# Performance work log

Hardware: AMD Instinct MI355X
Metric: run time of the kernel (lower is better)

Reference implementation:

```python
import jax, jax.numpy as jnp
import numpy as np

H = 16  # num_heads
D = 64  # depth per head


def setup_inputs() -> dict:
    key = jax.random.key(0)
    ks = jax.random.split(key, 9)
    hd = H * D
    s = 1.0 / np.sqrt(hd)
    return {
        "x": jax.random.normal(ks[0], (2, 2048, hd), dtype=jnp.float32),
        "wq_w": jax.random.normal(ks[1], (hd, hd), dtype=jnp.float32) * s,
        "wq_b": jnp.zeros((hd,), dtype=jnp.float32),
        "wk_w": jax.random.normal(ks[2], (hd, hd), dtype=jnp.float32) * s,
        "wk_b": jnp.zeros((hd,), dtype=jnp.float32),
        "wv_w": jax.random.normal(ks[3], (hd, hd), dtype=jnp.float32) * s,
        "wv_b": jnp.zeros((hd,), dtype=jnp.float32),
        "fc_w": jax.random.normal(ks[4], (hd, hd), dtype=jnp.float32) * s,
        "fc_b": jnp.zeros((hd,), dtype=jnp.float32),
    }


def reference(x, wq_w, wq_b, wk_w, wk_b, wv_w, wv_b, fc_w, fc_b):
    B, S, HD = x.shape
    # Linear layers (torch Linear: y = x @ W^T + b)
    q = x @ wq_w.T + wq_b
    k = x @ wk_w.T + wk_b
    v = x @ wv_w.T + wv_b
    # split heads -> [B, H, S, D]
    split = lambda t: t.reshape(B, S, H, D).transpose(0, 2, 1, 3)
    q, k, v = split(q), split(k), split(v)
    scale = 1.0 / jnp.sqrt(jnp.float32(D))
    logits = jnp.einsum("bhqd,bhkd->bhqk", q, k) * scale
    attn = jax.nn.softmax(logits, axis=-1)
    out = jnp.einsum("bhqk,bhkd->bhqd", attn, v)
    out = out.transpose(0, 2, 1, 3).reshape(B, S, HD)
    return out @ fc_w.T + fc_b
```

## Files before the change

### kernel.cpp

```cpp
#include <hip/hip_runtime.h>
#include <hip/hip_bf16.h>

typedef __hip_bfloat16 bf16;
typedef __attribute__((ext_vector_type(8))) short bf16x8;
typedef __attribute__((ext_vector_type(4))) float f32x4;
typedef __attribute__((ext_vector_type(16))) float f32x16;

static constexpr int SEQ = 2048;
static constexpr int HDIM = 1024;
static constexpr int NH = 16;
static constexpr int DH = 64;

__device__ __forceinline__ f32x4 mfma16(bf16x8 a, bf16x8 b, f32x4 c) {
  return __builtin_amdgcn_mfma_f32_16x16x32_bf16(a, b, c, 0, 0, 0);
}
__device__ __forceinline__ f32x16 mfma32(bf16x8 a, bf16x8 b, f32x16 c) {
  return __builtin_amdgcn_mfma_f32_32x32x16_bf16(a, b, c, 0, 0, 0);
}

__device__ __forceinline__ void gload_lds16(const bf16* g, bf16* l) {
  __builtin_amdgcn_global_load_lds(
      (const __attribute__((address_space(1))) void*)g,
      (__attribute__((address_space(3))) void*)l, 16, 0, 0);
}

__device__ __forceinline__ unsigned packbf(float a, float b) {
  unsigned short ua = __builtin_bit_cast(unsigned short, __float2bfloat16(a));
  unsigned short ub = __builtin_bit_cast(unsigned short, __float2bfloat16(b));
  return (unsigned)ua | ((unsigned)ub << 16);
}

__global__ __launch_bounds__(256) void cvt_bf16(const float* __restrict__ in,
                                                bf16* __restrict__ out, int n4) {
  int i = blockIdx.x * blockDim.x + threadIdx.x;
  if (i >= n4) return;
  float4 v = reinterpret_cast<const float4*>(in)[i];
  bf16 t[4] = {__float2bfloat16(v.x), __float2bfloat16(v.y),
               __float2bfloat16(v.z), __float2bfloat16(v.w)};
  reinterpret_cast<ushort4*>(out)[i] = *reinterpret_cast<ushort4*>(t);
}

__device__ __forceinline__ void gemm_core(const bf16* __restrict__ A,
                                          const bf16* __restrict__ W,
                                          int m0, int n0, int K,
                                          f32x4 (&acc)[4][4],
                                          bf16* As, bf16* Bs) {
  const int tid = threadIdx.x;
  const int w = tid >> 6, lane = tid & 63;
  const int wr = w >> 1, wc = w & 1;
  const int lr = lane & 15, lk = (lane >> 4) * 8;
  const int srow = lane >> 2, scol = (lane & 3) * 8;

  for (int kt = 0; kt < K; kt += 32) {
#pragma unroll
    for (int j = 0; j < 2; ++j) {
      int cidx = w * 2 + j;
      int r = cidx * 16 + srow;
      gload_lds16(A + (size_t)(m0 + r) * K + kt + scol, As + cidx * 512);
      gload_lds16(W + (size_t)(n0 + r) * K + kt + scol, Bs + cidx * 512);
    }
    __syncthreads();
    bf16x8 af[4], bw[4];
#pragma unroll
    for (int i = 0; i < 4; ++i)
      af[i] = *reinterpret_cast<const bf16x8*>(As + (wr * 64 + i * 16 + lr) * 32 + lk);
#pragma unroll
    for (int i = 0; i < 4; ++i)
      bw[i] = *reinterpret_cast<const bf16x8*>(Bs + (wc * 64 + i * 16 + lr) * 32 + lk);
#pragma unroll
    for (int r = 0; r < 4; ++r)
#pragma unroll
      for (int c = 0; c < 4; ++c)
        acc[r][c] = mfma16(af[r], bw[c], acc[r][c]);
    __syncthreads();
  }
}

__global__ __launch_bounds__(256)
void qkv_gemm(const bf16* __restrict__ xb,
              const bf16* __restrict__ wq, const bf16* __restrict__ wk,
              const bf16* __restrict__ wv,
              const float* __restrict__ bq, const float* __restrict__ bk,
              const float* __restrict__ bv,
              bf16* __restrict__ qd, bf16* __restrict__ kd, bf16* __restrict__ vT) {
  __shared__ bf16 As[128 * 32], Bs[128 * 32];
  const int z = blockIdx.z;
  const bf16* W = (z == 0) ? wq : (z == 1) ? wk : wv;
  const float* bias = (z == 0) ? bq : (z == 1) ? bk : bv;
  const float scale = (z == 0) ? 0.18033688011f : 1.0f;
  const int m0 = blockIdx.y * 128, n0 = blockIdx.x * 128;
  f32x4 acc[4][4] = {};
  gemm_core(xb, W, m0, n0, HDIM, acc, As, Bs);

  const int tid = threadIdx.x, w = tid >> 6, lane = tid & 63;
  const int wr = w >> 1, wc = w & 1;
  const int lr = lane & 15, rg = (lane >> 4) * 4;
#pragma unroll
  for (int r = 0; r < 4; ++r)
#pragma unroll
    for (int c = 0; c < 4; ++c) {
      int n = n0 + wc * 64 + c * 16 + lr;
      int h = n >> 6, d = n & 63;
      float bz = bias[n];
#pragma unroll
      for (int q = 0; q < 4; ++q) {
        int m = m0 + wr * 64 + r * 16 + rg + q;
        int b = m >> 11, s = m & 2047;
        bf16 val = __float2bfloat16((acc[r][c][q] + bz) * scale);
        if (z == 2)
          vT[(((size_t)(b * NH + h) * DH + d) << 11) + s] = val;
        else {
          bf16* dst = (z == 0) ? qd : kd;
          dst[(((size_t)(b * NH + h) * SEQ + s) << 6) + d] = val;
        }
      }
    }
}

__global__ __launch_bounds__(512, 4)
void attn_kernel(const bf16* __restrict__ Q, const bf16* __restrict__ K,
                 const bf16* __restrict__ vT, bf16* __restrict__ AO) {
  __shared__ float Olds[4][32][64];
  __shared__ float mlds[4][32], llds[4][32];
  __shared__ float als[8][32];
  __shared__ float af1[4][32], af2[4][32], li[4][32];

  const int lane = threadIdx.x & 63;
  const int wv = threadIdx.x >> 6;
  const int qw = wv & 3, kh = wv >> 2;
  const int l31 = lane & 31;
  const int hi = lane >> 5;
  const int bh = blockIdx.y;
  const int b = bh >> 4, h = bh & 15;
  const int q0 = blockIdx.x * 128 + qw * 32;

  const bf16* Qh = Q + (size_t)bh * SEQ * DH;
  const bf16* Kh = K + (size_t)bh * SEQ * DH;
  const bf16* Vh = vT + (size_t)bh * DH * SEQ;

  bf16x8 qf[4];
#pragma unroll
  for (int s = 0; s < 4; ++s)
    qf[s] = *reinterpret_cast<const bf16x8*>(
        Qh + (size_t)(q0 + l31) * DH + s * 16 + hi * 8);

  f32x16 o0 = {}, o1 = {};
  float m = -1e30f, l = 0.f;

  const int k_lo = kh << 10, k_hi = k_lo + 1024;
  for (int kt = k_lo; kt < k_hi; kt += 32) {
    f32x16 sacc = {};
#pragma unroll
    for (int s = 0; s < 4; ++s) {
      bf16x8 kf = *reinterpret_cast<const bf16x8*>(
          Kh + (size_t)(kt + l31) * DH + s * 16 + hi * 8);
      sacc = mfma32(kf, qf[s], sacc);
    }
    bf16x8 vf[2][2];
#pragma unroll
    for (int kk = 0; kk < 2; ++kk)
#pragma unroll
      for (int t = 0; t < 2; ++t)
        vf[kk][t] = *reinterpret_cast<const bf16x8*>(
            Vh + (size_t)(t * 32 + l31) * SEQ + kt + kk * 16 + hi * 8);

    float tm[8];
#pragma unroll
    for (int i = 0; i < 8; ++i) tm[i] = fmaxf(sacc[2 * i], sacc[2 * i + 1]);
#pragma unroll
    for (int i = 0; i < 4; ++i) tm[i] = fmaxf(tm[i], tm[i + 4]);
    float pmax = fmaxf(fmaxf(tm[0], tm[1]), fmaxf(tm[2], tm[3]));
    pmax = fmaxf(pmax, __shfl_xor(pmax, 32));

    if (__any(pmax > m + 11.5415603f)) {
      float mn = fmaxf(m, pmax);
      float al = exp2f(m - mn);
      m = mn; l *= al;
      if (lane < 32) als[wv][l31] = al;
      __builtin_amdgcn_wave_barrier();
#pragma unroll
      for (int r = 0; r < 16; ++r) {
        float a = als[wv][(r & 3) + 8 * (r >> 2) + 4 * hi];
        o0[r] *= a; o1[r] *= a;
      }
      __builtin_amdgcn_wave_barrier();
    }

    float p[16];
#pragma unroll
    for (int i = 0; i < 16; ++i) p[i] = exp2f(sacc[i] - m);
    float ts[8];
#pragma unroll
    for (int i = 0; i < 8; ++i) ts[i] = p[2 * i] + p[2 * i + 1];
#pragma unroll
    for (int i = 0; i < 4; ++i) ts[i] = ts[i] + ts[i + 4];
    float ps = (ts[0] + ts[1]) + (ts[2] + ts[3]);
    ps += __shfl_xor(ps, 32);
    l += ps;

    unsigned w[4][2], sw[4][2];
#pragma unroll
    for (int g = 0; g < 4; ++g) {
      w[g][0] = packbf(p[4 * g + 0], p[4 * g + 1]);
      w[g][1] = packbf(p[4 * g + 2], p[4 * g + 3]);
      sw[g][0] = __shfl_xor(w[g][0], 32);
      sw[g][1] = __shfl_xor(w[g][1], 32);
    }
#pragma unroll
    for (int kk = 0; kk < 2; ++kk) {
      union { unsigned u[4]; bf16x8 v; } fa;
      fa.u[0] = hi ? sw[2 * kk + 1][0] : w[2 * kk][0];
      fa.u[1] = hi ? sw[2 * kk + 1][1] : w[2 * kk][1];
      fa.u[2] = hi ? w[2 * kk + 1][0] : sw[2 * kk][0];
      fa.u[3] = hi ? w[2 * kk + 1][1] : sw[2 * kk][1];
      o0 = mfma32(fa.v, vf[kk][0], o0);
      o1 = mfma32(fa.v, vf[kk][1], o1);
    }
  }

  if (kh == 1) {
    if (lane < 32) { mlds[qw][l31] = m; llds[qw][l31] = l; }
#pragma unroll
    for (int r = 0; r < 16; ++r) {
      int q = (r & 3) + 8 * (r >> 2) + 4 * hi;
      Olds[qw][q][l31] = o0[r];
      Olds[qw][q][32 + l31] = o1[r];
    }
  }
  __syncthreads();
  if (kh == 0) {
    float m2 = mlds[qw][l31], l2 = llds[qw][l31];
    float mn = fmaxf(m, m2);
    float a1 = exp2f(m - mn), a2 = exp2f(m2 - mn);
    float inv = 1.0f / (l * a1 + l2 * a2);
    if (lane < 32) { af1[qw][l31] = a1; af2[qw][l31] = a2; li[qw][l31] = inv; }
    __builtin_amdgcn_wave_barrier();
#pragma unroll
    for (int r = 0; r < 16; ++r) {
      int q = (r & 3) + 8 * (r >> 2) + 4 * hi;
      float s1 = af1[qw][q], s2 = af2[qw][q], iv = li[qw][q];
      size_t row = (size_t)(b * SEQ + q0 + q) * HDIM + h * DH;
      AO[row + l31] =
          __float2bfloat16((o0[r] * s1 + Olds[qw][q][l31] * s2) * iv);
      AO[row + 32 + l31] =
          __float2bfloat16((o1[r] * s1 + Olds[qw][q][32 + l31] * s2) * iv);
    }
  }
}

__global__ __launch_bounds__(256)
void fc_gemm(const bf16* __restrict__ A, const bf16* __restrict__ W,
             const float* __restrict__ bias, float* __restrict__ out) {
  __shared__ bf16 As[128 * 32], Bs[128 * 32];
  const int m0 = blockIdx.y * 128, n0 = blockIdx.x * 128;
  f32x4 acc[4][4] = {};
  gemm_core(A, W, m0, n0, HDIM, acc, As, Bs);

  const int tid = threadIdx.x, w = tid >> 6, lane = tid & 63;
  const int wr = w >> 1, wc = w & 1;
  const int lr = lane & 15, rg = (lane >> 4) * 4;
#pragma unroll
  for (int r = 0; r < 4; ++r)
#pragma unroll
    for (int c = 0; c < 4; ++c) {
      int n = n0 + wc * 64 + c * 16 + lr;
      float bz = bias[n];
#pragma unroll
      for (int q = 0; q < 4; ++q) {
        int m = m0 + wr * 64 + r * 16 + rg + q;
        out[(size_t)m * HDIM + n] = acc[r][c][q] + bz;
      }
    }
}

extern "C" void kernel_launch(void* const* d_in, const int* in_sizes, int n_in,
                              void* d_out, int out_size, void* d_ws, size_t ws_size,
                              hipStream_t stream) {
  (void)in_sizes; (void)n_in; (void)out_size; (void)ws_size;
  const float* x  = (const float*)d_in[0];
  const float* wq = (const float*)d_in[1];
  const float* bq = (const float*)d_in[2];
  const float* wk = (const float*)d_in[3];
  const float* bk = (const float*)d_in[4];
  const float* wv = (const float*)d_in[5];
  const float* bv = (const float*)d_in[6];
  const float* wf = (const float*)d_in[7];
  const float* bf_ = (const float*)d_in[8];
  float* out = (float*)d_out;

  char* ws = (char*)d_ws;
  bf16* xb  = (bf16*)(ws);
  bf16* wqb = (bf16*)(ws + (8u << 20));
  bf16* wkb = (bf16*)(ws + (10u << 20));
  bf16* wvb = (bf16*)(ws + (12u << 20));
  bf16* wfb = (bf16*)(ws + (14u << 20));
  bf16* qd  = (bf16*)(ws + (16u << 20));
  bf16* kd  = (bf16*)(ws + (24u << 20));
  bf16* vT  = (bf16*)(ws + (32u << 20));
  bf16* ao  = (bf16*)(ws + (40u << 20));

  cvt_bf16<<<4096, 256, 0, stream>>>(x, xb, 1048576);
  cvt_bf16<<<1024, 256, 0, stream>>>(wq, wqb, 262144);
  cvt_bf16<<<1024, 256, 0, stream>>>(wk, wkb, 262144);
  cvt_bf16<<<1024, 256, 0, stream>>>(wv, wvb, 262144);
  cvt_bf16<<<1024, 256, 0, stream>>>(wf, wfb, 262144);

  qkv_gemm<<<dim3(8, 32, 3), 256, 0, stream>>>(xb, wqb, wkb, wvb, bq, bk, bv,
                                               qd, kd, vT);
  attn_kernel<<<dim3(16, 32), 512, 0, stream>>>(qd, kd, vT, ao);
  fc_gemm<<<dim3(8, 32), 256, 0, stream>>>(ao, wfb, bf_, out);
}
```

Before: 274.1 us.

## Use packed bf16 convert and permlane swap in attention; merge weight conversions

The four weight conversion launches become one launch that picks its input by blockIdx.z, removing three kernel launches. In the attention inner loop, the per-element bf16 packing and cross-half shuffles with selects are replaced by v_cvt_pk_bf16_f32 and v_permlane32_swap_b32 inline assembly. The row max is rebuilt from three-input max trees, and the K/V addresses now come from incremented pointers instead of per-iteration index maths. The gain is fewer VALU and cross-lane instructions per tile, at the cost of relying on gfx950-specific instructions and inline asm whose operand order must reproduce the previous fragment layout.

```diff
diff --git a/kernel.cpp b/kernel.cpp
--- a/kernel.cpp
+++ b/kernel.cpp
@@ -24,16 +24,43 @@
       (__attribute__((address_space(3))) void*)l, 16, 0, 0);
 }
 
-__device__ __forceinline__ unsigned packbf(float a, float b) {
-  unsigned short ua = __builtin_bit_cast(unsigned short, __float2bfloat16(a));
-  unsigned short ub = __builtin_bit_cast(unsigned short, __float2bfloat16(b));
-  return (unsigned)ua | ((unsigned)ub << 16);
+__device__ __forceinline__ unsigned cvtpk(float lo, float hi) {
+  unsigned r;
+  asm("v_cvt_pk_bf16_f32 %0, %1, %2" : "=v"(r) : "v"(lo), "v"(hi));
+  return r;
+}
+__device__ __forceinline__ void plswap(unsigned& a, unsigned& b) {
+  asm volatile("v_permlane32_swap_b32 %0, %1" : "+v"(a), "+v"(b));
+}
+__device__ __forceinline__ float xhalf_max(float x) {
+  return fmaxf(x, __shfl_xor(x, 32));
+}
+__device__ __forceinline__ float xhalf_sum(float x) {
+  return x + __shfl_xor(x, 32);
+}
+__device__ __forceinline__ float max3f(float a, float b, float c) {
+  return fmaxf(fmaxf(a, b), c);
 }
 
 __global__ __launch_bounds__(256) void cvt_bf16(const float* __restrict__ in,
                                                 bf16* __restrict__ out, int n4) {
   int i = blockIdx.x * blockDim.x + threadIdx.x;
   if (i >= n4) return;
+  float4 v = reinterpret_cast<const float4*>(in)[i];
+  bf16 t[4] = {__float2bfloat16(v.x), __float2bfloat16(v.y),
+               __float2bfloat16(v.z), __float2bfloat16(v.w)};
+  reinterpret_cast<ushort4*>(out)[i] = *reinterpret_cast<ushort4*>(t);
+}
+
+__global__ __launch_bounds__(256)
+void cvt_w4(const float* __restrict__ w0, const float* __restrict__ w1,
+            const float* __restrict__ w2, const float* __restrict__ w3,
+            bf16* __restrict__ o0, bf16* __restrict__ o1,
+            bf16* __restrict__ o2, bf16* __restrict__ o3) {
+  const int z = blockIdx.z;
+  const float* in = (z == 0) ? w0 : (z == 1) ? w1 : (z == 2) ? w2 : w3;
+  bf16* out = (z == 0) ? o0 : (z == 1) ? o1 : (z == 2) ? o2 : o3;
+  int i = blockIdx.x * blockDim.x + threadIdx.x;
   float4 v = reinterpret_cast<const float4*>(in)[i];
   bf16 t[4] = {__float2bfloat16(v.x), __float2bfloat16(v.y),
                __float2bfloat16(v.z), __float2bfloat16(v.w)};
@@ -147,30 +174,34 @@
   f32x16 o0 = {}, o1 = {};
   float m = -1e30f, l = 0.f;
 
-  const int k_lo = kh << 10, k_hi = k_lo + 1024;
-  for (int kt = k_lo; kt < k_hi; kt += 32) {
+  const int k_lo = kh << 10;
+  const bf16* kptr = Kh + (size_t)(k_lo + l31) * DH + hi * 8;
+  const bf16* vp0 = Vh + (size_t)l31 * SEQ + k_lo + hi * 8;
+  const bf16* vp1 = Vh + (size_t)(32 + l31) * SEQ + k_lo + hi * 8;
+
+  for (int it = 0; it < 32; ++it) {
     f32x16 sacc = {};
 #pragma unroll
     for (int s = 0; s < 4; ++s) {
-      bf16x8 kf = *reinterpret_cast<const bf16x8*>(
-          Kh + (size_t)(kt + l31) * DH + s * 16 + hi * 8);
+      bf16x8 kf = *reinterpret_cast<const bf16x8*>(kptr + s * 16);
       sacc = mfma32(kf, qf[s], sacc);
     }
+    kptr += 32 * DH;
     bf16x8 vf[2][2];
 #pragma unroll
-    for (int kk = 0; kk < 2; ++kk)
-#pragma unroll
-      for (int t = 0; t < 2; ++t)
-        vf[kk][t] = *reinterpret_cast<const bf16x8*>(
-            Vh + (size_t)(t * 32 + l31) * SEQ + kt + kk * 16 + hi * 8);
-
-    float tm[8];
-#pragma unroll
-    for (int i = 0; i < 8; ++i) tm[i] = fmaxf(sacc[2 * i], sacc[2 * i + 1]);
-#pragma unroll
-    for (int i = 0; i < 4; ++i) tm[i] = fmaxf(tm[i], tm[i + 4]);
-    float pmax = fmaxf(fmaxf(tm[0], tm[1]), fmaxf(tm[2], tm[3]));
-    pmax = fmaxf(pmax, __shfl_xor(pmax, 32));
+    for (int kk = 0; kk < 2; ++kk) {
+      vf[kk][0] = *reinterpret_cast<const bf16x8*>(vp0 + kk * 16);
+      vf[kk][1] = *reinterpret_cast<const bf16x8*>(vp1 + kk * 16);
+    }
+    vp0 += 32; vp1 += 32;
+
+    float t0 = max3f(sacc[0], sacc[1], sacc[2]);
+    float t1 = max3f(sacc[3], sacc[4], sacc[5]);
+    float t2 = max3f(sacc[6], sacc[7], sacc[8]);
+    float t3 = max3f(sacc[9], sacc[10], sacc[11]);
+    float t4 = max3f(sacc[12], sacc[13], sacc[14]);
+    float pmax = fmaxf(max3f(t0, t1, t2), max3f(t3, t4, sacc[15]));
+    pmax = xhalf_max(pmax);
 
     if (__any(pmax > m + 11.5415603f)) {
       float mn = fmaxf(m, pmax);
@@ -195,27 +226,24 @@
 #pragma unroll
     for (int i = 0; i < 4; ++i) ts[i] = ts[i] + ts[i + 4];
     float ps = (ts[0] + ts[1]) + (ts[2] + ts[3]);
-    ps += __shfl_xor(ps, 32);
-    l += ps;
-
-    unsigned w[4][2], sw[4][2];
-#pragma unroll
-    for (int g = 0; g < 4; ++g) {
-      w[g][0] = packbf(p[4 * g + 0], p[4 * g + 1]);
-      w[g][1] = packbf(p[4 * g + 2], p[4 * g + 3]);
-      sw[g][0] = __shfl_xor(w[g][0], 32);
-      sw[g][1] = __shfl_xor(w[g][1], 32);
-    }
-#pragma unroll
-    for (int kk = 0; kk < 2; ++kk) {
-      union { unsigned u[4]; bf16x8 v; } fa;
-      fa.u[0] = hi ? sw[2 * kk + 1][0] : w[2 * kk][0];
-      fa.u[1] = hi ? sw[2 * kk + 1][1] : w[2 * kk][1];
-      fa.u[2] = hi ? w[2 * kk + 1][0] : sw[2 * kk][0];
-      fa.u[3] = hi ? w[2 * kk + 1][1] : sw[2 * kk][1];
-      o0 = mfma32(fa.v, vf[kk][0], o0);
-      o1 = mfma32(fa.v, vf[kk][1], o1);
-    }
+    l += xhalf_sum(ps);
+
+    unsigned u00 = cvtpk(p[0], p[1]),  u01 = cvtpk(p[2], p[3]);
+    unsigned u10 = cvtpk(p[4], p[5]),  u11 = cvtpk(p[6], p[7]);
+    unsigned u20 = cvtpk(p[8], p[9]),  u21 = cvtpk(p[10], p[11]);
+    unsigned u30 = cvtpk(p[12], p[13]), u31 = cvtpk(p[14], p[15]);
+    plswap(u00, u10);
+    plswap(u01, u11);
+    plswap(u20, u30);
+    plswap(u21, u31);
+
+    union { unsigned u[4]; bf16x8 v; } fa0, fa1;
+    fa0.u[0] = u00; fa0.u[1] = u01; fa0.u[2] = u10; fa0.u[3] = u11;
+    fa1.u[0] = u20; fa1.u[1] = u21; fa1.u[2] = u30; fa1.u[3] = u31;
+    o0 = mfma32(fa0.v, vf[0][0], o0);
+    o1 = mfma32(fa0.v, vf[0][1], o1);
+    o0 = mfma32(fa1.v, vf[1][0], o0);
+    o1 = mfma32(fa1.v, vf[1][1], o1);
   }
 
   if (kh == 1) {
@@ -300,10 +328,8 @@
   bf16* ao  = (bf16*)(ws + (40u << 20));
 
   cvt_bf16<<<4096, 256, 0, stream>>>(x, xb, 1048576);
-  cvt_bf16<<<1024, 256, 0, stream>>>(wq, wqb, 262144);
-  cvt_bf16<<<1024, 256, 0, stream>>>(wk, wkb, 262144);
-  cvt_bf16<<<1024, 256, 0, stream>>>(wv, wvb, 262144);
-  cvt_bf16<<<1024, 256, 0, stream>>>(wf, wfb, 262144);
+  cvt_w4<<<dim3(1024, 1, 4), 256, 0, stream>>>(wq, wk, wv, wf,
+                                               wqb, wkb, wvb, wfb);
 
   qkv_gemm<<<dim3(8, 32, 3), 256, 0, stream>>>(xb, wqb, wkb, wvb, bq, bk, bv,
                                                qd, kd, vT);
```

Result: no change. 269.0 us (-1.9%).
